# Optimization experiments

Measured on AMD Instinct MI355X. Metric: run time of the kernel, lower is better.

## Reference

```python
import jax, jax.numpy as jnp
import numpy as np

N_NODES = 50000
NEG_SLOPE = 0.2


def gat_conv(x, src, dst, W, att_src, att_dst, bias, concat):
    # x: [N, F_in], W: [H*D, F_in], att_*: [H, D], bias: [H*D] or [D]
    N = x.shape[0]
    H, D = att_src.shape
    h = (x @ W.T).reshape(N, H, D)                      # [N, H, D]
    a_src = jnp.einsum('nhd,hd->nh', h, att_src)        # [N, H]
    a_dst = jnp.einsum('nhd,hd->nh', h, att_dst)        # [N, H]
    e = jax.nn.leaky_relu(a_src[src] + a_dst[dst], NEG_SLOPE)  # [E, H]
    # softmax over incoming edges of each destination node
    m = jax.ops.segment_max(e, dst, num_segments=N)     # [N, H]
    ex = jnp.exp(e - m[dst])
    denom = jax.ops.segment_sum(ex, dst, num_segments=N)
    alpha = ex / denom[dst]                             # [E, H]
    msg = alpha[:, :, None] * h[src]                    # [E, H, D]
    out = jax.ops.segment_sum(msg, dst, num_segments=N) # [N, H, D]
    out = out.reshape(N, H * D) if concat else out.mean(axis=1)
    return out + bias


def setup_inputs() -> dict:
    key = jax.random.key(0)
    ks = jax.random.split(key, 10)
    nfeat, nhid, nclass, heads = 256, 128, 40, 4
    d1 = nhid // heads  # 32
    E = 800000
    x = jax.random.normal(ks[0], (N_NODES, nfeat), dtype=jnp.float32)
    edge_index = jax.random.randint(ks[1], (2, E), 0, N_NODES, dtype=jnp.int64)
    s = 0.1
    W1 = jax.random.normal(ks[2], (heads * d1, nfeat), dtype=jnp.float32) * s
    att_src1 = jax.random.normal(ks[3], (heads, d1), dtype=jnp.float32) * s
    att_dst1 = jax.random.normal(ks[4], (heads, d1), dtype=jnp.float32) * s
    b1 = jnp.zeros((heads * d1,), dtype=jnp.float32)
    W2 = jax.random.normal(ks[5], (nclass, nhid), dtype=jnp.float32) * s
    att_src2 = jax.random.normal(ks[6], (1, nclass), dtype=jnp.float32) * s
    att_dst2 = jax.random.normal(ks[7], (1, nclass), dtype=jnp.float32) * s
    b2 = jnp.zeros((nclass,), dtype=jnp.float32)
    return {"x": x, "edge_index": edge_index, "W1": W1, "att_src1": att_src1,
            "att_dst1": att_dst1, "b1": b1, "W2": W2, "att_src2": att_src2,
            "att_dst2": att_dst2, "b2": b2}


def reference(x, edge_index, W1, att_src1, att_dst1, b1, W2, att_src2, att_dst2, b2):
    # PyG GATConv adds self-loops by default
    loops = jnp.arange(N_NODES, dtype=edge_index.dtype)
    src = jnp.concatenate([edge_index[0], loops])
    dst = jnp.concatenate([edge_index[1], loops])
    h = gat_conv(x, src, dst, W1, att_src1, att_dst1, b1, concat=True)
    h = jax.nn.relu(h)
    # dropout is identity in eval mode
    out = gat_conv(h, src, dst, W2, att_src2, att_dst2, b2, concat=True)
    return out
```

## Files before the change

kernel.cpp:

```cpp
#include <hip/hip_runtime.h>
#include <hip/hip_bf16.h>
#include <cstdint>
#include <cstddef>

#define N_NODES 50000
#define NEG_SLOPE 0.2f
#define NB 196
#define BIN_CHUNK 8192
#define SLICE_MAX 14336

typedef float floatx4 __attribute__((ext_vector_type(4)));
typedef short shortx8 __attribute__((ext_vector_type(8)));

__device__ __forceinline__ unsigned short f2b(float f) {
    union { float f; unsigned u; } v; v.f = f;
    unsigned u = v.u;
    return (unsigned short)((u + 0x7FFFu + ((u >> 16) & 1u)) >> 16);
}
__device__ __forceinline__ float b2f(unsigned short b) {
    union { unsigned u; float f; } v; v.u = ((unsigned)b) << 16;
    return v.f;
}

__global__ __launch_bounds__(256) void bucket_hist_kernel(
    const int* __restrict__ ei, int E0, int E, int* __restrict__ bhist) {
    __shared__ int h[NB];
    int t = threadIdx.x;
    for (int i = t; i < NB; i += 256) h[i] = 0;
    __syncthreads();
    int base = blockIdx.x * BIN_CHUNK;
    int end = min(base + BIN_CHUNK, E);
    for (int e = base + t; e < end; e += 256) {
        int d = (e < E0) ? ei[E0 + e] : (e - E0);
        atomicAdd(&h[d >> 8], 1);
    }
    __syncthreads();
    for (int i = t; i < NB; i += 256)
        if (h[i]) atomicAdd(&bhist[i], h[i]);
}

__global__ __launch_bounds__(256) void bucket_scan_kernel(
    const int* __restrict__ bhist, int* __restrict__ bbase,
    int* __restrict__ bcursor, int* __restrict__ rowptr, int E) {
    __shared__ int buf[256];
    int t = threadIdx.x;
    int v = (t < NB) ? bhist[t] : 0;
    int x = v;
    for (int off = 1; off < 256; off <<= 1) {
        buf[t] = x; __syncthreads();
        int y = (t >= off) ? buf[t - off] : 0;
        __syncthreads();
        x += y;
    }
    if (t < NB) {
        bbase[t] = x - v;
        bcursor[t] = x - v;
    }
    if (t == NB - 1) bbase[NB] = x;
    if (t == 0) rowptr[N_NODES] = E;
}

__global__ __launch_bounds__(256) void bin_kernel(
    const int* __restrict__ ei, int E0, int E,
    int* __restrict__ bcursor, unsigned int* __restrict__ ebuf) {
    __shared__ int h[NB];
    __shared__ int gbase[NB];
    int t = threadIdx.x;
    for (int i = t; i < NB; i += 256) h[i] = 0;
    __syncthreads();
    int base = blockIdx.x * BIN_CHUNK;
    int end = min(base + BIN_CHUNK, E);
    for (int e = base + t; e < end; e += 256) {
        int d = (e < E0) ? ei[E0 + e] : (e - E0);
        atomicAdd(&h[d >> 8], 1);
    }
    __syncthreads();
    for (int i = t; i < NB; i += 256) {
        int c = h[i];
        gbase[i] = c ? atomicAdd(&bcursor[i], c) : 0;
        h[i] = 0;
    }
    __syncthreads();
    for (int e = base + t; e < end; e += 256) {
        int s, d;
        if (e < E0) { s = ei[e]; d = ei[E0 + e]; }
        else        { s = e - E0; d = e - E0; }
        int b = d >> 8;
        int off = atomicAdd(&h[b], 1);
        ebuf[gbase[b] + off] = (unsigned)s | ((unsigned)(d & 255) << 16);
    }
}

__global__ __launch_bounds__(256) void build_kernel(
    const unsigned int* __restrict__ ebuf, const int* __restrict__ bbase,
    int* __restrict__ rowptr, int* __restrict__ csr_src) {
    __shared__ int h[256];
    __shared__ int lrp[257];
    __shared__ int stag[SLICE_MAX];
    int b = blockIdx.x, t = threadIdx.x;
    int e0 = bbase[b], e1 = bbase[b + 1];
    int cnt = e1 - e0;
    int n0 = b << 8;
    h[t] = 0;
    __syncthreads();
    for (int i = t; i < cnt; i += 256)
        atomicAdd(&h[ebuf[e0 + i] >> 16], 1);
    __syncthreads();
    int v = h[t], x = v;
    __shared__ int buf[256];
    for (int off = 1; off < 256; off <<= 1) {
        buf[t] = x; __syncthreads();
        int y = (t >= off) ? buf[t - off] : 0;
        __syncthreads();
        x += y;
    }
    lrp[t] = x - v;
    if (t == 255) lrp[256] = x;
    h[t] = 0;
    __syncthreads();
    int n = n0 + t;
    if (n < N_NODES) rowptr[n] = e0 + lrp[t];
    for (int i = t; i < cnt; i += 256) {
        unsigned int v2 = ebuf[e0 + i];
        int dloc = v2 >> 16;
        int off = atomicAdd(&h[dloc], 1);
        stag[lrp[dloc] + off] = (int)(v2 & 0xFFFFu);
    }
    __syncthreads();
    for (int i = t; i < cnt; i += 256) csr_src[e0 + i] = stag[i];
}

template <int BM, int BN, int NREAL, int KK, typename InT>
__global__ __launch_bounds__(256) void gemm_bf16_kernel(
    const InT* __restrict__ A, const float* __restrict__ B,
    unsigned short* __restrict__ Cb, int M) {
    const int BK = 64, LDK = 72;
    const int NT = BN / 16;
    __shared__ unsigned short As[BM * LDK];
    __shared__ unsigned short Bs[BN * LDK];
    const int t = threadIdx.x;
    const int wave = t >> 6, lane = t & 63;
    const int lrow = lane & 15, lkg = lane >> 4;
    const int bm = blockIdx.x * BM;

    floatx4 acc[NT] = {};

    for (int k0 = 0; k0 < KK; k0 += BK) {
        __syncthreads();
        if constexpr (sizeof(InT) == 4) {
            for (int i = t; i < BM * 16; i += 256) {
                int r = i >> 4, c4 = (i & 15) << 2;
                int gr = bm + r;
                float4 v = make_float4(0.f, 0.f, 0.f, 0.f);
                if (gr < M) v = *(const float4*)&A[(size_t)gr * KK + k0 + c4];
                int o = r * LDK + c4;
                As[o] = f2b(v.x); As[o + 1] = f2b(v.y);
                As[o + 2] = f2b(v.z); As[o + 3] = f2b(v.w);
            }
        } else {
            for (int i = t; i < BM * 8; i += 256) {
                int r = i >> 3, c8 = (i & 7) << 3;
                int gr = bm + r;
                shortx8 v = {};
                if (gr < M) v = *(const shortx8*)&A[(size_t)gr * KK + k0 + c8];
                *(shortx8*)&As[r * LDK + c8] = v;
            }
        }
        for (int i = t; i < BN * 16; i += 256) {
            int r = i >> 4, c4 = (i & 15) << 2;
            float4 v = make_float4(0.f, 0.f, 0.f, 0.f);
            if (r < NREAL) v = *(const float4*)&B[(size_t)r * KK + k0 + c4];
            int o = r * LDK + c4;
            Bs[o] = f2b(v.x); Bs[o + 1] = f2b(v.y);
            Bs[o + 2] = f2b(v.z); Bs[o + 3] = f2b(v.w);
        }
        __syncthreads();

        for (int ks = 0; ks < BK; ks += 32) {
            int kc = ks + lkg * 8;
            int row = wave * 16 + lrow;
            shortx8 a = *(const shortx8*)&As[row * LDK + kc];
#pragma unroll
            for (int nt = 0; nt < NT; nt++) {
                shortx8 b = *(const shortx8*)&Bs[(nt * 16 + lrow) * LDK + kc];
                acc[nt] = __builtin_amdgcn_mfma_f32_16x16x32_bf16(a, b, acc[nt], 0, 0, 0);
            }
        }
    }
#pragma unroll
    for (int nt = 0; nt < NT; nt++)
#pragma unroll
        for (int r = 0; r < 4; r++) {
            int row = bm + wave * 16 + lkg * 4 + r;
            int col = nt * 16 + lrow;
            if (row < M && col < NREAL)
                Cb[(size_t)row * NREAL + col] = f2b(acc[nt][r]);
        }
}

__global__ void att1_kernel(const unsigned short* __restrict__ h1b,
                            const float* __restrict__ att_src,
                            const float* __restrict__ att_dst,
                            float* __restrict__ a_src, float* __restrict__ a_dst,
                            int N) {
    int i = blockIdx.x * blockDim.x + threadIdx.x;
    if (i >= N * 4) return;
    int h = i & 3;
    const ushort4* hp = (const ushort4*)(h1b + (size_t)i * 32);
    const float4* as = (const float4*)(att_src + h * 32);
    const float4* ad = (const float4*)(att_dst + h * 32);
    float ssum = 0.f, dsum = 0.f;
#pragma unroll
    for (int j = 0; j < 8; j++) {
        ushort4 hv = hp[j];
        float4 av = as[j], dv = ad[j];
        float x0 = b2f(hv.x), x1 = b2f(hv.y), x2 = b2f(hv.z), x3 = b2f(hv.w);
        ssum += x0 * av.x + x1 * av.y + x2 * av.z + x3 * av.w;
        dsum += x0 * dv.x + x1 * dv.y + x2 * dv.z + x3 * dv.w;
    }
    a_src[i] = ssum;
    a_dst[i] = dsum;
}

__global__ void att2_kernel(const unsigned short* __restrict__ h2b,
                            const float* __restrict__ att_src,
                            const float* __restrict__ att_dst,
                            float* __restrict__ a_src, float* __restrict__ a_dst,
                            int N) {
    int n = blockIdx.x * blockDim.x + threadIdx.x;
    if (n >= N) return;
    const ushort4* hp = (const ushort4*)(h2b + (size_t)n * 40);
    const float4* as = (const float4*)att_src;
    const float4* ad = (const float4*)att_dst;
    float ssum = 0.f, dsum = 0.f;
#pragma unroll
    for (int j = 0; j < 10; j++) {
        ushort4 hv = hp[j];
        float4 av = as[j], dv = ad[j];
        float x0 = b2f(hv.x), x1 = b2f(hv.y), x2 = b2f(hv.z), x3 = b2f(hv.w);
        ssum += x0 * av.x + x1 * av.y + x2 * av.z + x3 * av.w;
        dsum += x0 * dv.x + x1 * dv.y + x2 * dv.z + x3 * dv.w;
    }
    a_src[n] = ssum;
    a_dst[n] = dsum;
}

__global__ __launch_bounds__(256) void agg1_kernel(
    const unsigned short* __restrict__ h1b, const float* __restrict__ a_src,
    const float* __restrict__ a_dst, const int* __restrict__ rowptr,
    const int* __restrict__ csr_src, const float* __restrict__ b1,
    unsigned short* __restrict__ zb, int N) {
    int wave = threadIdx.x >> 6, lane = threadIdx.x & 63;
    int n = blockIdx.x * 4 + wave;
    if (n >= N) return;
    int half = lane >> 5, pos = lane & 31, head = pos >> 3;
    float adn = a_dst[n * 4 + (lane & 3)];
    int beg = rowptr[n], deg = rowptr[n + 1] - beg;

    floatx4 acc = {0.f, 0.f, 0.f, 0.f};
    float den = 0.f;
    for (int c0 = 0; c0 < deg; c0 += 16) {
        int idx = c0 + (lane >> 2);
        int s_e = (idx < deg) ? csr_src[beg + idx] : 0;
        float l = a_src[(s_e << 2) + (lane & 3)] + adn;
        l = l > 0.f ? l : NEG_SLOPE * l;
        float w_e = (idx < deg) ? __expf(l) : 0.f;
        int cnt = min(16, deg - c0);
        if (cnt == 16) {
            int s_arr[8]; float w_arr[8]; ushort4 v_arr[8];
#pragma unroll
            for (int p = 0; p < 8; p++) {
                int el = (p << 1) + half;
                s_arr[p] = __shfl(s_e, el << 2);
                w_arr[p] = __shfl(w_e, (el << 2) + head);
            }
#pragma unroll
            for (int p = 0; p < 8; p++)
                v_arr[p] = *(const ushort4*)&h1b[(size_t)s_arr[p] * 128 + pos * 4];
#pragma unroll
            for (int p = 0; p < 8; p++) {
                float w = w_arr[p];
                den += w;
                acc.x += w * b2f(v_arr[p].x);
                acc.y += w * b2f(v_arr[p].y);
                acc.z += w * b2f(v_arr[p].z);
                acc.w += w * b2f(v_arr[p].w);
            }
        } else {
            int npair = (cnt + 1) >> 1;
            for (int p = 0; p < npair; p++) {
                int el = (p << 1) + half;
                int s = __shfl(s_e, el << 2);
                float w = __shfl(w_e, (el << 2) + head);
                ushort4 v = *(const ushort4*)&h1b[(size_t)s * 128 + pos * 4];
                den += w;
                acc.x += w * b2f(v.x);
                acc.y += w * b2f(v.y);
                acc.z += w * b2f(v.z);
                acc.w += w * b2f(v.w);
            }
        }
    }
    acc.x += __shfl_xor(acc.x, 32);
    acc.y += __shfl_xor(acc.y, 32);
    acc.z += __shfl_xor(acc.z, 32);
    acc.w += __shfl_xor(acc.w, 32);
    den   += __shfl_xor(den, 32);
    if (half == 0) {
        float inv = 1.f / den;
        float4 bb = *(const float4*)&b1[pos * 4];
        float o0 = fmaxf(acc.x * inv + bb.x, 0.f);
        float o1 = fmaxf(acc.y * inv + bb.y, 0.f);
        float o2 = fmaxf(acc.z * inv + bb.z, 0.f);
        float o3 = fmaxf(acc.w * inv + bb.w, 0.f);
        ushort4 r;
        r.x = f2b(o0); r.y = f2b(o1); r.z = f2b(o2); r.w = f2b(o3);
        *(ushort4*)&zb[(size_t)n * 128 + pos * 4] = r;
    }
}

__global__ __launch_bounds__(256) void agg2_kernel(
    const unsigned short* __restrict__ h2b, const float* __restrict__ a_src,
    const float* __restrict__ a_dst, const int* __restrict__ rowptr,
    const int* __restrict__ csr_src, const float* __restrict__ b2,
    float* __restrict__ out, int N) {
    int wave = threadIdx.x >> 6, lane = threadIdx.x & 63;
    int n = blockIdx.x * 4 + wave;
    if (n >= N) return;
    int half = lane >> 5, pos = lane & 31;
    float adn = a_dst[n];
    int beg = rowptr[n], deg = rowptr[n + 1] - beg;

    float2 acc = {0.f, 0.f};
    float den = 0.f;
    for (int c0 = 0; c0 < deg; c0 += 64) {
        int idx = c0 + lane;
        int s_e = (idx < deg) ? csr_src[beg + idx] : 0;
        float l = a_src[s_e] + adn;
        l = l > 0.f ? l : NEG_SLOPE * l;
        float w_e = (idx < deg) ? __expf(l) : 0.f;
        int cnt = min(64, deg - c0);
        int npair = (cnt + 1) >> 1;
        int p = 0;
        for (; p + 8 <= npair; p += 8) {
            int s_arr[8]; float w_arr[8]; ushort2 v_arr[8];
#pragma unroll
            for (int q = 0; q < 8; q++) {
                int el = ((p + q) << 1) + half;
                s_arr[q] = __shfl(s_e, el);
                w_arr[q] = __shfl(w_e, el);
            }
            if (pos < 20) {
#pragma unroll
                for (int q = 0; q < 8; q++)
                    v_arr[q] = *(const ushort2*)&h2b[(size_t)s_arr[q] * 40 + pos * 2];
            }
#pragma unroll
            for (int q = 0; q < 8; q++) {
                float w = w_arr[q];
                den += w;
                if (pos < 20) {
                    acc.x += w * b2f(v_arr[q].x);
                    acc.y += w * b2f(v_arr[q].y);
                }
            }
        }
        for (; p < npair; p++) {
            int el = (p << 1) + half;
            int s = __shfl(s_e, el);
            float w = __shfl(w_e, el);
            den += w;
            if (pos < 20) {
                ushort2 v = *(const ushort2*)&h2b[(size_t)s * 40 + pos * 2];
                acc.x += w * b2f(v.x);
                acc.y += w * b2f(v.y);
            }
        }
    }
    acc.x += __shfl_xor(acc.x, 32);
    acc.y += __shfl_xor(acc.y, 32);
    den   += __shfl_xor(den, 32);
    if (half == 0 && pos < 20) {
        float inv = 1.f / den;
        float2 bb = *(const float2*)&b2[pos * 2];
        float2 o;
        o.x = acc.x * inv + bb.x;
        o.y = acc.y * inv + bb.y;
        *(float2*)&out[(size_t)n * 40 + pos * 2] = o;
    }
}

extern "C" void kernel_launch(void* const* d_in, const int* in_sizes, int n_in,
                              void* d_out, int out_size, void* d_ws, size_t ws_size,
                              hipStream_t stream) {
    const float* x        = (const float*)d_in[0];
    const int*   ei       = (const int*)d_in[1];
    const float* W1       = (const float*)d_in[2];
    const float* att_src1 = (const float*)d_in[3];
    const float* att_dst1 = (const float*)d_in[4];
    const float* b1       = (const float*)d_in[5];
    const float* W2       = (const float*)d_in[6];
    const float* att_src2 = (const float*)d_in[7];
    const float* att_dst2 = (const float*)d_in[8];
    const float* b2       = (const float*)d_in[9];
    float* out = (float*)d_out;

    const int N  = N_NODES;
    const int E0 = in_sizes[1] / 2;
    const int E  = E0 + N;
    const int NBLK = (E + BIN_CHUNK - 1) / BIN_CHUNK;

    char* ws = (char*)d_ws;
    unsigned short* h1b = (unsigned short*)(ws + 0);
    unsigned short* zb  = (unsigned short*)(ws + 12800000);
    unsigned short* h2b = (unsigned short*)(ws + 25600000);
    float* a_src1 = (float*)(ws + 29600000);
    float* a_dst1 = (float*)(ws + 30400000);
    float* a_src2 = (float*)(ws + 31200000);
    float* a_dst2 = (float*)(ws + 31400000);
    int*   rowptr = (int*)(ws + 31600000);
    int*   bhist  = (int*)(ws + 31800192);
    int*   bbase  = (int*)(ws + 31801088);
    int*   bcursor= (int*)(ws + 31801984);
    unsigned int* ebuf = (unsigned int*)(ws + 31802880);
    int*   csr_src= (int*)(ws + 35202880);

    hipMemsetAsync(bhist, 0, NB * sizeof(int), stream);

    bucket_hist_kernel<<<NBLK, 256, 0, stream>>>(ei, E0, E, bhist);
    bucket_scan_kernel<<<1, 256, 0, stream>>>(bhist, bbase, bcursor, rowptr, E);
    bin_kernel<<<NBLK, 256, 0, stream>>>(ei, E0, E, bcursor, ebuf);
    build_kernel<<<NB, 256, 0, stream>>>(ebuf, bbase, rowptr, csr_src);

    gemm_bf16_kernel<64, 128, 128, 256, float>
        <<<(N + 63) / 64, 256, 0, stream>>>(x, W1, h1b, N);
    att1_kernel<<<(N * 4 + 255) / 256, 256, 0, stream>>>(h1b, att_src1, att_dst1, a_src1, a_dst1, N);
    agg1_kernel<<<(N + 3) / 4, 256, 0, stream>>>(h1b, a_src1, a_dst1, rowptr, csr_src, b1, zb, N);

    gemm_bf16_kernel<64, 48, 40, 128, unsigned short>
        <<<(N + 63) / 64, 256, 0, stream>>>(zb, W2, h2b, N);
    att2_kernel<<<(N + 255) / 256, 256, 0, stream>>>(h2b, att_src2, att_dst2, a_src2, a_dst2, N);
    agg2_kernel<<<(N + 3) / 4, 256, 0, stream>>>(h2b, a_src2, a_dst2, rowptr, csr_src, b2, out, N);
}
```

Before: 249.7 us.

## Precompute per-edge exp attention weights in separate kernels before aggregation

```diff
diff --git a/kernel.cpp b/kernel.cpp
--- a/kernel.cpp
+++ b/kernel.cpp
@@ -93,10 +93,10 @@
 
 __global__ __launch_bounds__(256) void build_kernel(
     const unsigned int* __restrict__ ebuf, const int* __restrict__ bbase,
-    int* __restrict__ rowptr, int* __restrict__ csr_src) {
+    int* __restrict__ rowptr, unsigned int* __restrict__ csrp) {
     __shared__ int h[256];
     __shared__ int lrp[257];
-    __shared__ int stag[SLICE_MAX];
+    __shared__ unsigned int stag[SLICE_MAX];
     int b = blockIdx.x, t = threadIdx.x;
     int e0 = bbase[b], e1 = bbase[b + 1];
     int cnt = e1 - e0;
@@ -124,10 +124,10 @@
         unsigned int v2 = ebuf[e0 + i];
         int dloc = v2 >> 16;
         int off = atomicAdd(&h[dloc], 1);
-        stag[lrp[dloc] + off] = (int)(v2 & 0xFFFFu);
-    }
-    __syncthreads();
-    for (int i = t; i < cnt; i += 256) csr_src[e0 + i] = stag[i];
+        stag[lrp[dloc] + off] = v2;
+    }
+    __syncthreads();
+    for (int i = t; i < cnt; i += 256) csrp[e0 + i] = stag[i];
 }
 
 template <int BM, int BN, int NREAL, int KK, typename InT>
@@ -245,61 +245,85 @@
     a_dst[n] = dsum;
 }
 
+__global__ __launch_bounds__(256) void edgew1_kernel(
+    const unsigned int* __restrict__ csrp, const int* __restrict__ bbase,
+    const float* __restrict__ a_src, const float* __restrict__ a_dst,
+    float* __restrict__ wexp) {
+    int b = blockIdx.x;
+    int i0 = bbase[b] * 4, i1 = bbase[b + 1] * 4;
+    int dbase = b << 10;
+    for (int i = i0 + blockIdx.y * 256 + threadIdx.x; i < i1; i += 256 * 8) {
+        unsigned v = csrp[i >> 2];
+        int h = i & 3;
+        int s = (int)(v & 0xFFFFu);
+        int dloc = (int)(v >> 16);
+        float a = a_src[(s << 2) + h] + a_dst[dbase + (dloc << 2) + h];
+        a = a > 0.f ? a : NEG_SLOPE * a;
+        wexp[i] = __expf(a);
+    }
+}
+
+__global__ __launch_bounds__(256) void edgew2_kernel(
+    const unsigned int* __restrict__ csrp, const int* __restrict__ bbase,
+    const float* __restrict__ a_src, const float* __restrict__ a_dst,
+    float* __restrict__ wexp) {
+    int b = blockIdx.x;
+    int i0 = bbase[b], i1 = bbase[b + 1];
+    int dbase = b << 8;
+    for (int i = i0 + blockIdx.y * 256 + threadIdx.x; i < i1; i += 256 * 2) {
+        unsigned v = csrp[i];
+        float a = a_src[v & 0xFFFFu] + a_dst[dbase + (v >> 16)];
+        a = a > 0.f ? a : NEG_SLOPE * a;
+        wexp[i] = __expf(a);
+    }
+}
+
 __global__ __launch_bounds__(256) void agg1_kernel(
-    const unsigned short* __restrict__ h1b, const float* __restrict__ a_src,
-    const float* __restrict__ a_dst, const int* __restrict__ rowptr,
-    const int* __restrict__ csr_src, const float* __restrict__ b1,
-    unsigned short* __restrict__ zb, int N) {
+    const unsigned short* __restrict__ h1b, const float* __restrict__ wexp,
+    const unsigned int* __restrict__ csrp, const int* __restrict__ rowptr,
+    const float* __restrict__ b1, unsigned short* __restrict__ zb, int N) {
     int wave = threadIdx.x >> 6, lane = threadIdx.x & 63;
     int n = blockIdx.x * 4 + wave;
     if (n >= N) return;
     int half = lane >> 5, pos = lane & 31, head = pos >> 3;
-    float adn = a_dst[n * 4 + (lane & 3)];
     int beg = rowptr[n], deg = rowptr[n + 1] - beg;
+
+    const unsigned int* cp = csrp + beg;
+    const float* wp = wexp + ((size_t)beg << 2) + head;
 
     floatx4 acc = {0.f, 0.f, 0.f, 0.f};
     float den = 0.f;
-    for (int c0 = 0; c0 < deg; c0 += 16) {
-        int idx = c0 + (lane >> 2);
-        int s_e = (idx < deg) ? csr_src[beg + idx] : 0;
-        float l = a_src[(s_e << 2) + (lane & 3)] + adn;
-        l = l > 0.f ? l : NEG_SLOPE * l;
-        float w_e = (idx < deg) ? __expf(l) : 0.f;
-        int cnt = min(16, deg - c0);
-        if (cnt == 16) {
-            int s_arr[8]; float w_arr[8]; ushort4 v_arr[8];
-#pragma unroll
-            for (int p = 0; p < 8; p++) {
-                int el = (p << 1) + half;
-                s_arr[p] = __shfl(s_e, el << 2);
-                w_arr[p] = __shfl(w_e, (el << 2) + head);
-            }
-#pragma unroll
-            for (int p = 0; p < 8; p++)
-                v_arr[p] = *(const ushort4*)&h1b[(size_t)s_arr[p] * 128 + pos * 4];
-#pragma unroll
-            for (int p = 0; p < 8; p++) {
-                float w = w_arr[p];
-                den += w;
-                acc.x += w * b2f(v_arr[p].x);
-                acc.y += w * b2f(v_arr[p].y);
-                acc.z += w * b2f(v_arr[p].z);
-                acc.w += w * b2f(v_arr[p].w);
-            }
-        } else {
-            int npair = (cnt + 1) >> 1;
-            for (int p = 0; p < npair; p++) {
-                int el = (p << 1) + half;
-                int s = __shfl(s_e, el << 2);
-                float w = __shfl(w_e, (el << 2) + head);
-                ushort4 v = *(const ushort4*)&h1b[(size_t)s * 128 + pos * 4];
-                den += w;
-                acc.x += w * b2f(v.x);
-                acc.y += w * b2f(v.y);
-                acc.z += w * b2f(v.z);
-                acc.w += w * b2f(v.w);
-            }
-        }
+    int i = half;
+    for (; i + 14 < deg; i += 16) {
+        unsigned s_arr[8]; float w_arr[8]; ushort4 v_arr[8];
+#pragma unroll
+        for (int q = 0; q < 8; q++) {
+            int e = i + (q << 1);
+            s_arr[q] = cp[e] & 0xFFFFu;
+            w_arr[q] = wp[e << 2];
+        }
+#pragma unroll
+        for (int q = 0; q < 8; q++)
+            v_arr[q] = *(const ushort4*)&h1b[(size_t)s_arr[q] * 128 + pos * 4];
+#pragma unroll
+        for (int q = 0; q < 8; q++) {
+            float w = w_arr[q];
+            den += w;
+            acc.x += w * b2f(v_arr[q].x);
+            acc.y += w * b2f(v_arr[q].y);
+            acc.z += w * b2f(v_arr[q].z);
+            acc.w += w * b2f(v_arr[q].w);
+        }
+    }
+    for (; i < deg; i += 2) {
+        unsigned s = cp[i] & 0xFFFFu;
+        float w = wp[i << 2];
+        ushort4 v = *(const ushort4*)&h1b[(size_t)s * 128 + pos * 4];
+        den += w;
+        acc.x += w * b2f(v.x);
+        acc.y += w * b2f(v.y);
+        acc.z += w * b2f(v.z);
+        acc.w += w * b2f(v.w);
     }
     acc.x += __shfl_xor(acc.x, 32);
     acc.y += __shfl_xor(acc.y, 32);
@@ -320,61 +344,52 @@
 }
 
 __global__ __launch_bounds__(256) void agg2_kernel(
-    const unsigned short* __restrict__ h2b, const float* __restrict__ a_src,
-    const float* __restrict__ a_dst, const int* __restrict__ rowptr,
-    const int* __restrict__ csr_src, const float* __restrict__ b2,
-    float* __restrict__ out, int N) {
+    const unsigned short* __restrict__ h2b, const float* __restrict__ wexp,
+    const unsigned int* __restrict__ csrp, const int* __restrict__ rowptr,
+    const float* __restrict__ b2, float* __restrict__ out, int N) {
     int wave = threadIdx.x >> 6, lane = threadIdx.x & 63;
     int n = blockIdx.x * 4 + wave;
     if (n >= N) return;
     int half = lane >> 5, pos = lane & 31;
-    float adn = a_dst[n];
     int beg = rowptr[n], deg = rowptr[n + 1] - beg;
+
+    const unsigned int* cp = csrp + beg;
+    const float* wp = wexp + beg;
 
     float2 acc = {0.f, 0.f};
     float den = 0.f;
-    for (int c0 = 0; c0 < deg; c0 += 64) {
-        int idx = c0 + lane;
-        int s_e = (idx < deg) ? csr_src[beg + idx] : 0;
-        float l = a_src[s_e] + adn;
-        l = l > 0.f ? l : NEG_SLOPE * l;
-        float w_e = (idx < deg) ? __expf(l) : 0.f;
-        int cnt = min(64, deg - c0);
-        int npair = (cnt + 1) >> 1;
-        int p = 0;
-        for (; p + 8 <= npair; p += 8) {
-            int s_arr[8]; float w_arr[8]; ushort2 v_arr[8];
-#pragma unroll
-            for (int q = 0; q < 8; q++) {
-                int el = ((p + q) << 1) + half;
-                s_arr[q] = __shfl(s_e, el);
-                w_arr[q] = __shfl(w_e, el);
-            }
-            if (pos < 20) {
-#pragma unroll
-                for (int q = 0; q < 8; q++)
-                    v_arr[q] = *(const ushort2*)&h2b[(size_t)s_arr[q] * 40 + pos * 2];
-            }
-#pragma unroll
-            for (int q = 0; q < 8; q++) {
-                float w = w_arr[q];
-                den += w;
-                if (pos < 20) {
-                    acc.x += w * b2f(v_arr[q].x);
-                    acc.y += w * b2f(v_arr[q].y);
-                }
-            }
-        }
-        for (; p < npair; p++) {
-            int el = (p << 1) + half;
-            int s = __shfl(s_e, el);
-            float w = __shfl(w_e, el);
+    int i = half;
+    for (; i + 14 < deg; i += 16) {
+        unsigned s_arr[8]; float w_arr[8]; ushort2 v_arr[8];
+#pragma unroll
+        for (int q = 0; q < 8; q++) {
+            int e = i + (q << 1);
+            s_arr[q] = cp[e] & 0xFFFFu;
+            w_arr[q] = wp[e];
+        }
+        if (pos < 20) {
+#pragma unroll
+            for (int q = 0; q < 8; q++)
+                v_arr[q] = *(const ushort2*)&h2b[(size_t)s_arr[q] * 40 + pos * 2];
+        }
+#pragma unroll
+        for (int q = 0; q < 8; q++) {
+            float w = w_arr[q];
             den += w;
             if (pos < 20) {
-                ushort2 v = *(const ushort2*)&h2b[(size_t)s * 40 + pos * 2];
-                acc.x += w * b2f(v.x);
-                acc.y += w * b2f(v.y);
+                acc.x += w * b2f(v_arr[q].x);
+                acc.y += w * b2f(v_arr[q].y);
             }
+        }
+    }
+    for (; i < deg; i += 2) {
+        unsigned s = cp[i] & 0xFFFFu;
+        float w = wp[i];
+        den += w;
+        if (pos < 20) {
+            ushort2 v = *(const ushort2*)&h2b[(size_t)s * 40 + pos * 2];
+            acc.x += w * b2f(v.x);
+            acc.y += w * b2f(v.y);
         }
     }
     acc.x += __shfl_xor(acc.x, 32);
@@ -423,22 +438,26 @@
     int*   bbase  = (int*)(ws + 31801088);
     int*   bcursor= (int*)(ws + 31801984);
     unsigned int* ebuf = (unsigned int*)(ws + 31802880);
-    int*   csr_src= (int*)(ws + 35202880);
+    unsigned int* csrp = (unsigned int*)(ws + 35202880);
+    float* wexp1  = (float*)(ws + 38602880);
+    float* wexp2  = (float*)(ws + 52202880);
 
     hipMemsetAsync(bhist, 0, NB * sizeof(int), stream);
 
     bucket_hist_kernel<<<NBLK, 256, 0, stream>>>(ei, E0, E, bhist);
     bucket_scan_kernel<<<1, 256, 0, stream>>>(bhist, bbase, bcursor, rowptr, E);
     bin_kernel<<<NBLK, 256, 0, stream>>>(ei, E0, E, bcursor, ebuf);
-    build_kernel<<<NB, 256, 0, stream>>>(ebuf, bbase, rowptr, csr_src);
+    build_kernel<<<NB, 256, 0, stream>>>(ebuf, bbase, rowptr, csrp);
 
     gemm_bf16_kernel<64, 128, 128, 256, float>
         <<<(N + 63) / 64, 256, 0, stream>>>(x, W1, h1b, N);
     att1_kernel<<<(N * 4 + 255) / 256, 256, 0, stream>>>(h1b, att_src1, att_dst1, a_src1, a_dst1, N);
-    agg1_kernel<<<(N + 3) / 4, 256, 0, stream>>>(h1b, a_src1, a_dst1, rowptr, csr_src, b1, zb, N);
+    edgew1_kernel<<<dim3(NB, 8), 256, 0, stream>>>(csrp, bbase, a_src1, a_dst1, wexp1);
+    agg1_kernel<<<(N + 3) / 4, 256, 0, stream>>>(h1b, wexp1, csrp, rowptr, b1, zb, N);
 
     gemm_bf16_kernel<64, 48, 40, 128, unsigned short>
         <<<(N + 63) / 64, 256, 0, stream>>>(zb, W2, h2b, N);
     att2_kernel<<<(N + 255) / 256, 256, 0, stream>>>(h2b, att_src2, att_dst2, a_src2, a_dst2, N);
-    agg2_kernel<<<(N + 3) / 4, 256, 0, stream>>>(h2b, a_src2, a_dst2, rowptr, csr_src, b2, out, N);
-}
+    edgew2_kernel<<<dim3(NB, 2), 256, 0, stream>>>(csrp, bbase, a_src2, a_dst2, wexp2);
+    agg2_kernel<<<(N + 3) / 4, 256, 0, stream>>>(h2b, wexp2, csrp, rowptr, b2, out, N);
+}
```

Result: slower. 273.4 us (+9.5%).
